# Kernel tuning notes

Hardware: AMD Instinct MI355X
Metric: run time of the kernel (lower is better)

## Reference

```python
import jax, jax.numpy as jnp
import numpy as np

B, N, E, D, F_IN, EDGE_DIM, VN = 128, 500, 1048576, 128, 5, 2, 10
NEG_FEAT = 0.01   # torch F.leaky_relu default
NEG_ATT = 0.2     # GAT attention slope


def _gat_layer(h_in, src, dst, edge_attr, W, b, a_src, a_dst, a_edge, We, n_nodes):
    # Edge-feature GAT conv: per-edge attention over (src, dst, edge) then
    # softmax-normalized scatter-aggregate onto destination nodes.
    h = h_in @ W                                  # [N, d]
    e = edge_attr @ We                            # [E, d] projected edge features
    logits = jax.nn.leaky_relu((h @ a_src)[src] + (h @ a_dst)[dst] + e @ a_edge,
                               negative_slope=NEG_ATT)    # [E]
    # segment softmax over incoming edges of each dst node
    m = jax.ops.segment_max(logits, dst, num_segments=n_nodes)
    ex = jnp.exp(logits - m[dst])
    denom = jax.ops.segment_sum(ex, dst, num_segments=n_nodes)
    alpha = ex / (denom[dst] + 1e-16)             # [E]
    msg = h[src] + e                              # [E, d]
    out = jax.ops.segment_sum(alpha[:, None] * msg, dst, num_segments=n_nodes)
    return out + b


def setup_inputs() -> dict:
    key = jax.random.key(0)
    ks = jax.random.split(key, 20)
    s = 0.05
    return {
        'x': jax.random.normal(ks[0], (B * N, F_IN), jnp.float32),
        'edge_index': jax.random.randint(ks[1], (2, E), 0, B * N, jnp.int64 if jax.config.jax_enable_x64 else jnp.int32).astype(jnp.int32),
        'edge_attr': jax.random.uniform(ks[2], (E, EDGE_DIM), jnp.float32),
        'curr_v_node_id': jax.random.randint(ks[3], (B,), 0, VN).astype(jnp.int32),
        'v_graph_embedding': jax.random.normal(ks[4], (B, D), jnp.float32),
        'v_node_dense_embeddings': jax.random.normal(ks[5], (B, VN, D), jnp.float32),
        'p_W': jax.random.normal(ks[6], (F_IN, D), jnp.float32) * s,
        'p_b': jnp.zeros((D,), jnp.float32),
        'Ws': jax.random.normal(ks[7], (4, D, D), jnp.float32) * s,
        'bs': jnp.zeros((4, D), jnp.float32),
        'a_srcs': jax.random.normal(ks[8], (4, D), jnp.float32) * s,
        'a_dsts': jax.random.normal(ks[9], (4, D), jnp.float32) * s,
        'a_edges': jax.random.normal(ks[10], (4, D), jnp.float32) * s,
        'Wes': jax.random.normal(ks[11], (4, EDGE_DIM, D), jnp.float32) * s,
        'W5': jax.random.normal(ks[12], (D, 1), jnp.float32) * s,
        'b5': jnp.zeros((1,), jnp.float32),
        'a_src5': jax.random.normal(ks[13], (1,), jnp.float32) * s,
        'a_dst5': jax.random.normal(ks[14], (1,), jnp.float32) * s,
        'a_edge5': jax.random.normal(ks[15], (1,), jnp.float32) * s,
        'We5': jax.random.normal(ks[16], (EDGE_DIM, 1), jnp.float32) * s,
    }


def reference(x, edge_index, edge_attr, curr_v_node_id, v_graph_embedding,
              v_node_dense_embeddings, p_W, p_b, Ws, bs, a_srcs, a_dsts,
              a_edges, Wes, W5, b5, a_src5, a_dst5, a_edge5, We5):
    n_nodes = x.shape[0]
    src, dst = edge_index[0], edge_index[1]
    # gather current v-node embedding: [B, D]
    curr_emb = v_node_dense_embeddings[jnp.arange(B), curr_v_node_id]
    # linear + leaky_relu then broadcast-add of graph/node context
    h = jax.nn.leaky_relu(x @ p_W + p_b, negative_slope=NEG_FEAT)  # [B*N, D]
    h = h.reshape(B, N, D) + v_graph_embedding[:, None, :] + curr_emb[:, None, :]
    h = h.reshape(B * N, D)
    # 4 hidden edge-feature GAT layers (128 -> 128) with leaky_relu
    for l in range(4):
        h = _gat_layer(h, src, dst, edge_attr, Ws[l], bs[l], a_srcs[l],
                       a_dsts[l], a_edges[l], Wes[l], n_nodes)
        h = jax.nn.leaky_relu(h, negative_slope=NEG_FEAT)
    # output layer (128 -> 1), no activation
    h = _gat_layer(h, src, dst, edge_attr, W5, b5, a_src5, a_dst5, a_edge5,
                   We5, n_nodes)                    # [B*N, 1]
    return h.reshape(B, N)
```

## Files before the change

### kernel.cpp

```cpp
#include <hip/hip_runtime.h>
#include <hip/hip_bf16.h>

#define BB   128
#define NN   500
#define NV   64000
#define EE   1048576
#define DD   128
#define FIN  5
#define VNN  10
#define NBUK 250
#define BCAP 8192

typedef unsigned int   uint32;
typedef unsigned short u16b;
typedef __attribute__((ext_vector_type(8))) short short8;
typedef __attribute__((ext_vector_type(4))) float float4v;

#define P_ASRC  0
#define P_ADST  512
#define P_WE    1024
#define P_BIAS  2048
#define P_W5    2560
#define P_CVEC  2688
#define P_SC5   2700
#define P_TOT   2816

static __device__ __forceinline__ float bf2f(__hip_bfloat16 v) { return __bfloat162float(v); }
static __device__ __forceinline__ float lo2f(uint32 u) { return __uint_as_float(u << 16); }
static __device__ __forceinline__ float hi2f(uint32 u) { return __uint_as_float(u & 0xFFFF0000u); }
static __device__ __forceinline__ uint32 f2bf_bits(float f) {
    uint32 u = __float_as_uint(f);
    return (u + 0x7FFFu + ((u >> 16) & 1u)) >> 16;
}
static __device__ __forceinline__ uint32 pack2(float a, float b) {
    return (f2bf_bits(a) & 0xFFFFu) | (f2bf_bits(b) << 16);
}
static __device__ __forceinline__ float ldf(const void* p, int i, int flag) {
    return flag ? ((const float*)p)[i] : bf2f(((const __hip_bfloat16*)p)[i]);
}

__global__ void sniff_kernel(const unsigned short* __restrict__ p16, int* __restrict__ FLAG) {
    __shared__ int sHigh, sZero;
    if (threadIdx.x == 0) { sHigh = 0; sZero = 0; }
    __syncthreads();
    unsigned short v = p16[2 * threadIdx.x];
    if (v >= 0x8000u) atomicOr(&sHigh, 1);
    if (v == 0)       atomicAdd(&sZero, 1);
    __syncthreads();
    if (threadIdx.x == 0) FLAG[0] = (sHigh || sZero >= 128) ? 1 : 0;
}

__global__ void zero_out_kernel(void* __restrict__ out, const int* __restrict__ FLAG, float tag) {
    int i = blockIdx.x * blockDim.x + threadIdx.x;
    if (i >= NV) return;
    float v = (i == 0) ? tag : 0.f;
    if (FLAG[0]) ((float*)out)[i] = v;
    else         ((u16b*)out)[i] = (u16b)f2bf_bits(v);
}

__global__ void prep_kernel(const void* __restrict__ Wes, const void* __restrict__ aeg,
                            const void* __restrict__ We5, const void* __restrict__ ae5,
                            const void* __restrict__ asr, const void* __restrict__ ads,
                            const void* __restrict__ bs, const void* __restrict__ W5,
                            const void* __restrict__ b5, const void* __restrict__ as5,
                            const void* __restrict__ ad5, const int* __restrict__ FLAG,
                            float* __restrict__ PAR) {
    const int flag = FLAG[0];
    if (blockIdx.x == 0) {
        for (int i = threadIdx.x; i < 512; i += 256) PAR[P_ASRC + i] = ldf(asr, i, flag);
    } else if (blockIdx.x == 1) {
        for (int i = threadIdx.x; i < 512; i += 256) PAR[P_ADST + i] = ldf(ads, i, flag);
    } else if (blockIdx.x == 2) {
        for (int i = threadIdx.x; i < 1024; i += 256) PAR[P_WE + i] = ldf(Wes, i, flag);
    } else if (blockIdx.x == 3) {
        for (int i = threadIdx.x; i < 512; i += 256) PAR[P_BIAS + i] = ldf(bs, i, flag);
    } else if (blockIdx.x == 4) {
        int tid = threadIdx.x;
        if (tid < 128) {
            PAR[P_W5 + tid] = ldf(W5, tid, flag);
        } else if (tid < 136) {
            int l = (tid - 128) >> 1, r = (tid - 128) & 1;
            float s = 0.f;
            for (int ch = 0; ch < DD; ++ch)
                s += ldf(Wes, l * 256 + r * DD + ch, flag) * ldf(aeg, l * DD + ch, flag);
            PAR[P_CVEC + l * 2 + r] = s;
        } else if (tid == 136) {
            float ae = ldf(ae5, 0, flag);
            float w0 = ldf(We5, 0, flag), w1 = ldf(We5, 1, flag);
            PAR[P_CVEC + 8] = w0 * ae; PAR[P_CVEC + 9] = w1 * ae;
            PAR[P_CVEC + 10] = w0;     PAR[P_CVEC + 11] = w1;
            PAR[P_SC5 + 0] = ldf(b5, 0, flag);
            PAR[P_SC5 + 1] = ldf(as5, 0, flag);
            PAR[P_SC5 + 2] = ldf(ad5, 0, flag);
        }
    }
}

__global__ __launch_bounds__(256) void prepack_kernel(const void* __restrict__ Ws,
                                                      const int* __restrict__ FLAG,
                                                      u16b* __restrict__ WB) {
    const int flag = FLAG[0];
    int t = blockIdx.x * 256 + threadIdx.x;
    int lane = t & 63;
    int frag = t >> 6;
    int nchunk = frag & 7, kblk = (frag >> 3) & 3, l = frag >> 5;
    int n = nchunk * 16 + (lane & 15);
    int kbase = kblk * 32 + (lane >> 4) * 8;
#pragma unroll
    for (int j = 0; j < 8; ++j) {
        int idx = l * 16384 + (kbase + j) * 128 + n;
        u16b bits = flag ? (u16b)f2bf_bits(((const float*)Ws)[idx])
                         : ((const u16b*)Ws)[idx];
        WB[(size_t)t * 8 + j] = bits;
    }
}

__global__ __launch_bounds__(256) void proj_kernel(
        const void* __restrict__ x, const void* __restrict__ pW,
        const void* __restrict__ pb, const int* __restrict__ curr,
        const void* __restrict__ vge, const void* __restrict__ vnd,
        const int* __restrict__ FLAG, uint32* __restrict__ H) {
    const int flag = FLAG[0];
    const int n = blockIdx.x * 4 + (threadIdx.x >> 6);
    const int lane = threadIdx.x & 63;
    const int b = n / NN;
    int cv = curr[b]; if ((unsigned)cv >= VNN) cv = 0;
    float xv[FIN];
#pragma unroll
    for (int k = 0; k < FIN; ++k) xv[k] = ldf(x, n * FIN + k, flag);
    const int ch = lane * 2;
    float s0 = ldf(pb, ch, flag), s1 = ldf(pb, ch + 1, flag);
#pragma unroll
    for (int k = 0; k < FIN; ++k) {
        s0 = fmaf(xv[k], ldf(pW, k * DD + ch, flag), s0);
        s1 = fmaf(xv[k], ldf(pW, k * DD + ch + 1, flag), s1);
    }
    s0 = (s0 > 0.f) ? s0 : 0.01f * s0;
    s1 = (s1 > 0.f) ? s1 : 0.01f * s1;
    s0 += ldf(vge, b * DD + ch, flag) + ldf(vnd, (b * VNN + cv) * DD + ch, flag);
    s1 += ldf(vge, b * DD + ch + 1, flag) + ldf(vnd, (b * VNN + cv) * DD + ch + 1, flag);
    H[(size_t)n * 64 + lane] = pack2(s0, s1);
}

__global__ void init_kernel(int* __restrict__ gcur, int* __restrict__ counts) {
    int t = blockIdx.x * 256 + threadIdx.x;
    if (t < NBUK) gcur[t] = t * BCAP;
    if (t < 512) counts[NV + t] = 0;
}

__global__ __launch_bounds__(256) void bucketize_kernel(
        const int* __restrict__ src, const int* __restrict__ dst,
        const void* __restrict__ eaP, const int* __restrict__ FLAG,
        int* __restrict__ gcur, uint32* __restrict__ bukx, uint32* __restrict__ buky) {
    __shared__ int cnt[256];
    __shared__ int cur[256];
    const int flag = FLAG[0];
    const int t = threadIdx.x;
    const int e0 = blockIdx.x * 4096;
    cnt[t] = 0;
    __syncthreads();
    int d[16];
#pragma unroll
    for (int i = 0; i < 16; ++i) {
        d[i] = dst[e0 + i * 256 + t];
        if ((unsigned)d[i] >= NV) d[i] = -1;
        if (d[i] >= 0) atomicAdd(&cnt[d[i] >> 8], 1);
    }
    __syncthreads();
    if (t < NBUK) {
        int c = cnt[t];
        cur[t] = c ? atomicAdd(&gcur[t], c) : 0;
    }
    __syncthreads();
#pragma unroll
    for (int i = 0; i < 16; ++i) {
        if (d[i] < 0) continue;
        int e = e0 + i * 256 + t;
        int b = d[i] >> 8;
        int s = src[e];
        if ((unsigned)s >= NV) s = 0;
        uint32 eb;
        if (flag) { float2 v = ((const float2*)eaP)[e]; eb = pack2(v.x, v.y); }
        else      eb = ((const uint32*)eaP)[e];
        int p = atomicAdd(&cur[b], 1);
        if (p < (b + 1) * BCAP) {
            bukx[p] = (uint32)((s & 0xFFFF) | ((d[i] & 255) << 16));
            buky[p] = eb;
        }
    }
}

__global__ __launch_bounds__(256) void bcount_kernel(
        const uint32* __restrict__ bukx, const int* __restrict__ gcur,
        int* __restrict__ counts) {
    __shared__ int c[256];
    const int b = blockIdx.x, t = threadIdx.x;
    c[t] = 0;
    __syncthreads();
    const int base = b * BCAP;
    int cnt = gcur[b] - base;
    if (cnt > BCAP) cnt = BCAP;
    for (int i = t; i < cnt; i += 256)
        atomicAdd(&c[(bukx[base + i] >> 16) & 255], 1);
    __syncthreads();
    counts[b * 256 + t] = c[t];
}

__global__ __launch_bounds__(256) void scan1_kernel(const int* __restrict__ counts,
                                                    int* __restrict__ row_ptr,
                                                    int* __restrict__ partials) {
    __shared__ int sdata[256];
    int tid = threadIdx.x;
    int4 v = ((const int4*)counts)[blockIdx.x * 256 + tid];
    int sum = v.x + v.y + v.z + v.w;
    sdata[tid] = sum;
    __syncthreads();
    int acc = sum;
    for (int off = 1; off < 256; off <<= 1) {
        int t = (tid >= off) ? sdata[tid - off] : 0;
        __syncthreads();
        acc += t;
        sdata[tid] = acc;
        __syncthreads();
    }
    int excl = acc - sum;
    int base = blockIdx.x * 1024 + tid * 4;
    int run = excl;
    if (base + 0 <= NV) row_ptr[base + 0] = run; run += v.x;
    if (base + 1 <= NV) row_ptr[base + 1] = run; run += v.y;
    if (base + 2 <= NV) row_ptr[base + 2] = run; run += v.z;
    if (base + 3 <= NV) row_ptr[base + 3] = run;
    if (tid == 255) partials[blockIdx.x] = acc;
}

__global__ __launch_bounds__(64) void scan2_kernel(const int* __restrict__ partials,
                                                   int* __restrict__ boff, int nb) {
    int lane = threadIdx.x;
    int v = (lane < nb) ? partials[lane] : 0;
    int orig = v;
#pragma unroll
    for (int off = 1; off < 64; off <<= 1) {
        int t = __shfl_up(v, off, 64);
        if (lane >= off) v += t;
    }
    boff[lane] = v - orig;
}

__global__ __launch_bounds__(256) void scan3_kernel(int* __restrict__ row_ptr,
                                                    const int* __restrict__ boff) {
    int add = boff[blockIdx.x];
    int base = blockIdx.x * 1024 + threadIdx.x * 4;
#pragma unroll
    for (int j = 0; j < 4; ++j) {
        int i = base + j;
        if (i <= NV) row_ptr[i] += add;
    }
}

__global__ __launch_bounds__(256) void bscatter_kernel(
        const uint32* __restrict__ bukx, const uint32* __restrict__ buky,
        const int* __restrict__ gcur, const int* __restrict__ row_ptr,
        int* __restrict__ csr_src, uint32* __restrict__ csr_ea) {
    __shared__ int cur[256];
    const int b = blockIdx.x, t = threadIdx.x;
    cur[t] = row_ptr[b * 256 + t];
    __syncthreads();
    const int base = b * BCAP;
    int cnt = gcur[b] - base;
    if (cnt > BCAP) cnt = BCAP;
    for (int i = t; i < cnt; i += 256) {
        uint32 x = bukx[base + i];
        uint32 y = buky[base + i];
        int p = atomicAdd(&cur[(x >> 16) & 255], 1);
        csr_src[p] = (int)(x & 0xFFFFu);
        csr_ea[p] = y;
    }
}

__global__ __launch_bounds__(256) void gemm_kernel(
        const uint32* __restrict__ Hu, const u16b* __restrict__ WBl,
        const float* __restrict__ PARl, uint32* __restrict__ HWu,
        float* __restrict__ ssrc, float* __restrict__ sdst) {
    __shared__ float hs[64 * 129];
    __shared__ float pp[512];
    const int tid = threadIdx.x;
    const int lane = tid & 63;
    const int wave = tid >> 6;
    const int quad = lane >> 4;
    const int n0 = blockIdx.x * 64;
    const int m = n0 + wave * 16 + (lane & 15);

    const u16b* hrow = (const u16b*)Hu + (size_t)m * 128;
    short8 a0 = *(const short8*)(hrow + 0  + quad * 8);
    short8 a1 = *(const short8*)(hrow + 32 + quad * 8);
    short8 a2 = *(const short8*)(hrow + 64 + quad * 8);
    short8 a3 = *(const short8*)(hrow + 96 + quad * 8);

#pragma unroll
    for (int nt = 0; nt < 8; ++nt) {
        const u16b* bbase = WBl + ((size_t)nt * 512 + lane * 8);
        short8 b0 = *(const short8*)(bbase + 0 * 4096);
        short8 b1 = *(const short8*)(bbase + 1 * 4096);
        short8 b2 = *(const short8*)(bbase + 2 * 4096);
        short8 b3 = *(const short8*)(bbase + 3 * 4096);
        float4v acc = {0.f, 0.f, 0.f, 0.f};
        acc = __builtin_amdgcn_mfma_f32_16x16x32_bf16(a0, b0, acc, 0, 0, 0);
        acc = __builtin_amdgcn_mfma_f32_16x16x32_bf16(a1, b1, acc, 0, 0, 0);
        acc = __builtin_amdgcn_mfma_f32_16x16x32_bf16(a2, b2, acc, 0, 0, 0);
        acc = __builtin_amdgcn_mfma_f32_16x16x32_bf16(a3, b3, acc, 0, 0, 0);
#pragma unroll
        for (int r = 0; r < 4; ++r)
            hs[(wave * 16 + quad * 4 + r) * 129 + nt * 16 + (lane & 15)] = acc[r];
    }
    __syncthreads();

    {
        const int mn = tid & 63, cg = tid >> 6;
        const float* Asr = PARl + P_ASRC;
        const float* Ads = PARl + P_ADST;
        const float* row = hs + mn * 129 + cg * 32;
        float ps = 0.f, pd = 0.f;
#pragma unroll
        for (int j = 0; j < 32; ++j) {
            float v = row[j];
            ps = fmaf(v, Asr[cg * 32 + j], ps);
            pd = fmaf(v, Ads[cg * 32 + j], pd);
        }
        pp[tid] = ps; pp[256 + tid] = pd;
    }
    __syncthreads();
    if (tid < 64) {
        ssrc[n0 + tid] = pp[tid] + pp[64 + tid] + pp[128 + tid] + pp[192 + tid];
        sdst[n0 + tid] = pp[256 + tid] + pp[320 + tid] + pp[384 + tid] + pp[448 + tid];
    }

#pragma unroll
    for (int i = 0; i < 4; ++i) {
        int flat = i * 2048 + tid * 8;
        int n = flat >> 7, c = flat & 127;
        const float* p = hs + n * 129 + c;
        uint4 v;
        v.x = pack2(p[0], p[1]); v.y = pack2(p[2], p[3]);
        v.z = pack2(p[4], p[5]); v.w = pack2(p[6], p[7]);
        *(uint4*)(HWu + (size_t)(n0 + n) * 64 + c / 2) = v;
    }
}

__global__ __launch_bounds__(256) void agg_kernel(
        const uint32* __restrict__ HWu, const float* __restrict__ ssrc,
        const float* __restrict__ sdst, const int* __restrict__ csr_src,
        const uint32* __restrict__ csr_ea, const int* __restrict__ row_ptr,
        const float* __restrict__ PAR, int layer, uint32* __restrict__ HoutU,
        float* __restrict__ hw5out, int wantw5) {
    const int lane = threadIdx.x & 63;
    const int n = blockIdx.x * 4 + (threadIdx.x >> 6);
    const int begin = __builtin_amdgcn_readfirstlane(row_ptr[n]);
    const int deg   = __builtin_amdgcn_readfirstlane(row_ptr[n + 1]) - begin;
    const float c0 = PAR[P_CVEC + 2 * layer], c1 = PAR[P_CVEC + 2 * layer + 1];
    const float sd = sdst[n];

    int   sv = 0;
    uint32 eb = 0;
    float L = -3.4e38f;
    if (lane < deg) {
        sv = csr_src[begin + lane];
        eb = csr_ea[begin + lane];
        L = fmaf(hi2f(eb), c1, fmaf(lo2f(eb), c0, ssrc[sv] + sd));
        L = (L > 0.f) ? L : 0.2f * L;
    }
    float m = L;
    for (int j0 = 64; j0 < deg; j0 += 64) {
        int j = j0 + lane;
        if (j < deg) {
            int s2 = csr_src[begin + j];
            uint32 e2 = csr_ea[begin + j];
            float L2 = fmaf(hi2f(e2), c1, fmaf(lo2f(e2), c0, ssrc[s2] + sd));
            L2 = (L2 > 0.f) ? L2 : 0.2f * L2;
            m = fmaxf(m, L2);
        }
    }
#pragma unroll
    for (int o = 32; o; o >>= 1) m = fmaxf(m, __shfl_xor(m, o, 64));

    float ex = (lane < deg) ? __expf(L - m) : 0.f;
    float dsum = ex, sx = ex * lo2f(eb), sy = ex * hi2f(eb);
    for (int j0 = 64; j0 < deg; j0 += 64) {
        int j = j0 + lane;
        if (j < deg) {
            int s2 = csr_src[begin + j];
            uint32 e2 = csr_ea[begin + j];
            float L2 = fmaf(hi2f(e2), c1, fmaf(lo2f(e2), c0, ssrc[s2] + sd));
            L2 = (L2 > 0.f) ? L2 : 0.2f * L2;
            float x2 = __expf(L2 - m);
            dsum += x2; sx = fmaf(x2, lo2f(e2), sx); sy = fmaf(x2, hi2f(e2), sy);
        }
    }
#pragma unroll
    for (int o = 32; o; o >>= 1) {
        dsum += __shfl_xor(dsum, o, 64);
        sx   += __shfl_xor(sx, o, 64);
        sy   += __shfl_xor(sy, o, 64);
    }

    const int dmain = (deg < 64) ? deg : 64;
    const uint32 exu = __float_as_uint(ex);
    float acc0 = 0.f, acc1 = 0.f;
    int jj = 0;
    for (; jj + 8 <= dmain; jj += 8) {
        int s8[8]; float e8[8]; uint32 hv[8];
#pragma unroll
        for (int q = 0; q < 8; ++q) {
            s8[q] = __builtin_amdgcn_readlane(sv, jj + q);
            e8[q] = __uint_as_float(__builtin_amdgcn_readlane((int)exu, jj + q));
        }
#pragma unroll
        for (int q = 0; q < 8; ++q) hv[q] = HWu[(size_t)s8[q] * 64 + lane];
#pragma unroll
        for (int q = 0; q < 8; ++q) {
            acc0 = fmaf(e8[q], lo2f(hv[q]), acc0);
            acc1 = fmaf(e8[q], hi2f(hv[q]), acc1);
        }
    }
    for (; jj < dmain; ++jj) {
        int s = __builtin_amdgcn_readlane(sv, jj);
        float e1v = __uint_as_float(__builtin_amdgcn_readlane((int)exu, jj));
        uint32 hb = HWu[(size_t)s * 64 + lane];
        acc0 = fmaf(e1v, lo2f(hb), acc0);
        acc1 = fmaf(e1v, hi2f(hb), acc1);
    }
    for (jj = 64; jj < deg; ++jj) {
        int s = csr_src[begin + jj];
        uint32 e2 = csr_ea[begin + jj];
        float L2 = fmaf(hi2f(e2), c1, fmaf(lo2f(e2), c0, ssrc[s] + sd));
        L2 = (L2 > 0.f) ? L2 : 0.2f * L2;
        float x2 = __expf(L2 - m);
        uint32 hb = HWu[(size_t)s * 64 + lane];
        acc0 = fmaf(x2, lo2f(hb), acc0);
        acc1 = fmaf(x2, hi2f(hb), acc1);
    }

    const int ch = lane * 2;
    const float* WEl = PAR + P_WE + layer * 256;
    const float inv = 1.f / (dsum + 1e-16f);
    const float* Bl = PAR + P_BIAS + layer * DD;
    float t0 = fmaf(sy, WEl[DD + ch],     fmaf(sx, WEl[ch],     acc0));
    float t1 = fmaf(sy, WEl[DD + ch + 1], fmaf(sx, WEl[ch + 1], acc1));
    float o0 = fmaf(t0, inv, Bl[ch]);
    float o1 = fmaf(t1, inv, Bl[ch + 1]);
    o0 = (o0 > 0.f) ? o0 : 0.01f * o0;
    o1 = (o1 > 0.f) ? o1 : 0.01f * o1;
    HoutU[(size_t)n * 64 + lane] = pack2(o0, o1);

    if (wantw5) {
        float p = o0 * PAR[P_W5 + ch] + o1 * PAR[P_W5 + ch + 1];
#pragma unroll
        for (int o = 32; o; o >>= 1) p += __shfl_xor(p, o, 64);
        if (lane == 0) hw5out[n] = p;
    }
}

__global__ __launch_bounds__(256) void final_kernel(
        const float* __restrict__ hw5, const int* __restrict__ csr_src,
        const uint32* __restrict__ csr_ea, const int* __restrict__ row_ptr,
        const float* __restrict__ PAR, const int* __restrict__ FLAG,
        void* __restrict__ out) {
    const int flag = FLAG[0];
    int lane = threadIdx.x & 63;
    int n = blockIdx.x * 4 + (threadIdx.x >> 6);
    int begin = __builtin_amdgcn_readfirstlane(row_ptr[n]);
    int deg   = __builtin_amdgcn_readfirstlane(row_ptr[n + 1]) - begin;
    float c50 = PAR[P_CVEC + 8], c51 = PAR[P_CVEC + 9];
    float ce0 = PAR[P_CVEC + 10], ce1 = PAR[P_CVEC + 11];
    float b5v = PAR[P_SC5], a5s = PAR[P_SC5 + 1];
    float hd = PAR[P_SC5 + 2] * hw5[n];

    float m = -3.4e38f;
    for (int j0 = 0; j0 < deg; j0 += 64) {
        int j = j0 + lane;
        if (j < deg) {
            int s = csr_src[begin + j];
            uint32 eb = csr_ea[begin + j];
            float L = fmaf(hi2f(eb), c51, fmaf(lo2f(eb), c50, fmaf(a5s, hw5[s], hd)));
            L = (L > 0.f) ? L : 0.2f * L;
            m = fmaxf(m, L);
        }
    }
#pragma unroll
    for (int o = 32; o; o >>= 1) m = fmaxf(m, __shfl_xor(m, o, 64));

    float dsum = 0.f, msum = 0.f;
    for (int j0 = 0; j0 < deg; j0 += 64) {
        int j = j0 + lane;
        if (j < deg) {
            int s = csr_src[begin + j];
            uint32 eb = csr_ea[begin + j];
            float hs5 = hw5[s];
            float L = fmaf(hi2f(eb), c51, fmaf(lo2f(eb), c50, fmaf(a5s, hs5, hd)));
            L = (L > 0.f) ? L : 0.2f * L;
            float ex = __expf(L - m);
            dsum += ex;
            msum = fmaf(ex, hs5 + fmaf(hi2f(eb), ce1, lo2f(eb) * ce0), msum);
        }
    }
#pragma unroll
    for (int o = 32; o; o >>= 1) {
        dsum += __shfl_xor(dsum, o, 64);
        msum += __shfl_xor(msum, o, 64);
    }
    if (lane == 0) {
        float r = msum / (dsum + 1e-16f) + b5v;
        if (flag) ((float*)out)[n] = r;
        else      ((u16b*)out)[n] = (u16b)f2bf_bits(r);
    }
}

extern "C" void kernel_launch(void* const* d_in, const int* in_sizes, int n_in,
                              void* d_out, int out_size, void* d_ws, size_t ws_size,
                              hipStream_t stream) {
    const void* x   = d_in[0];
    const int*  ei  = (const int*)d_in[1];
    const void* ea  = d_in[2];
    const int*  cur = (const int*)d_in[3];
    const void* vge = d_in[4];
    const void* vnd = d_in[5];
    const void* pW  = d_in[6];
    const void* pb  = d_in[7];
    const void* Ws  = d_in[8];
    const void* bs  = d_in[9];
    const void* asr = d_in[10];
    const void* ads = d_in[11];
    const void* aeg = d_in[12];
    const void* Wes = d_in[13];
    const void* W5  = d_in[14];
    const void* b5  = d_in[15];
    const void* as5 = d_in[16];
    const void* ad5 = d_in[17];
    const void* ae5 = d_in[18];
    const void* We5 = d_in[19];
    (void)in_sizes; (void)n_in; (void)out_size;

    const int* e_src = ei;
    const int* e_dst = ei + EE;

    size_t off = 0;
    char* base = (char*)d_ws;
    auto carve = [&](size_t bytes) {
        void* p = base + off;
        off += (bytes + 255) & ~(size_t)255;
        return p;
    };
    int*    FLAG   = (int*)carve(256);
    float*  PAR    = (float*)carve((size_t)P_TOT * 4);
    u16b*   WB     = (u16b*)carve(4 * DD * DD * 2);
    uint32* H0     = (uint32*)carve((size_t)NV * DD * 2);
    uint32* H1     = (uint32*)carve((size_t)NV * DD * 2);
    float*  SS     = (float*)carve(NV * 4);
    float*  SD     = (float*)carve(NV * 4);
    float*  HW5v   = (float*)carve(NV * 4);
    int*    COUNTS = (int*)carve(65536 * 4);
    int*    ROWPTR = (int*)carve(65536 * 4);
    int*    GCUR   = (int*)carve(256 * 4);
    int*    PART   = (int*)carve(256 * 4);
    int*    BOFF   = (int*)carve(256 * 4);
    int*    CSRS   = (int*)carve((size_t)EE * 4);
    uint32* CSREA  = (uint32*)carve((size_t)EE * 4);
    size_t need = off;

    uint32* BUKX = H1;
    uint32* BUKY = H1 + (size_t)NBUK * BCAP;

    sniff_kernel<<<1, 256, 0, stream>>>((const unsigned short*)ea, FLAG);

    if (need > ws_size) {
        zero_out_kernel<<<(NV + 255) / 256, 256, 0, stream>>>(
            d_out, FLAG, (float)(ws_size >> 20));
        return;
    }

    prep_kernel<<<5, 256, 0, stream>>>(Wes, aeg, We5, ae5, asr, ads, bs,
                                       W5, b5, as5, ad5, FLAG, PAR);
    prepack_kernel<<<32, 256, 0, stream>>>(Ws, FLAG, WB);
    proj_kernel<<<NV / 4, 256, 0, stream>>>(x, pW, pb, cur, vge, vnd, FLAG, H0);

    init_kernel<<<2, 256, 0, stream>>>(GCUR, COUNTS);
    bucketize_kernel<<<EE / 4096, 256, 0, stream>>>(e_src, e_dst, ea, FLAG,
                                                    GCUR, BUKX, BUKY);
    bcount_kernel<<<NBUK, 256, 0, stream>>>(BUKX, GCUR, COUNTS);
    scan1_kernel<<<63, 256, 0, stream>>>(COUNTS, ROWPTR, PART);
    scan2_kernel<<<1, 64, 0, stream>>>(PART, BOFF, 63);
    scan3_kernel<<<63, 256, 0, stream>>>(ROWPTR, BOFF);
    bscatter_kernel<<<NBUK, 256, 0, stream>>>(BUKX, BUKY, GCUR, ROWPTR,
                                              CSRS, CSREA);

    for (int l = 0; l < 4; ++l) {
        gemm_kernel<<<NV / 64, 256, 0, stream>>>(
            H0, WB + (size_t)l * 16384, PAR + l * DD, H1, SS, SD);
        agg_kernel<<<NV / 4, 256, 0, stream>>>(
            H1, SS, SD, CSRS, CSREA, ROWPTR, PAR, l, H0, HW5v, (l == 3) ? 1 : 0);
    }

    final_kernel<<<NV / 4, 256, 0, stream>>>(HW5v, CSRS, CSREA, ROWPTR, PAR,
                                             FLAG, d_out);
}
```

Before: 464.6 us.

## Split GAT aggregation into attention and channel-sliced gather with sliced H layout

Hidden features are stored as 8 channel slices of 16 channels each, so every node row within a slice is 32 bytes. The fused aggregation kernel is split in two. An attention kernel computes the normalized alpha per edge, stores it as fp16 packed beside the source index, and writes the edge-attribute sums per node. A gather kernel launched per slice then reads 8 edges at a time with 8 lanes per edge. The intent is a smaller working set per slice for better cache hit rates on the random source gathers. In exchange it adds a kernel launch per layer, extra edge-array traffic, fp16 alpha precision loss, and atomics for hw5.

```diff
diff --git a/kernel.cpp b/kernel.cpp
--- a/kernel.cpp
+++ b/kernel.cpp
@@ -1,5 +1,6 @@
 #include <hip/hip_runtime.h>
 #include <hip/hip_bf16.h>
+#include <hip/hip_fp16.h>
 
 #define BB   128
 #define NN   500
@@ -25,6 +26,8 @@
 #define P_SC5   2700
 #define P_TOT   2816
 
+#define HIDXU(s, n, u) (((size_t)(s) * NV + (n)) * 8 + (u))
+
 static __device__ __forceinline__ float bf2f(__hip_bfloat16 v) { return __bfloat162float(v); }
 static __device__ __forceinline__ float lo2f(uint32 u) { return __uint_as_float(u << 16); }
 static __device__ __forceinline__ float hi2f(uint32 u) { return __uint_as_float(u & 0xFFFF0000u); }
@@ -37,6 +40,9 @@
 }
 static __device__ __forceinline__ float ldf(const void* p, int i, int flag) {
     return flag ? ((const float*)p)[i] : bf2f(((const __hip_bfloat16*)p)[i]);
+}
+static __device__ __forceinline__ float a2f(uint32 al) {
+    return __half2float(__ushort_as_half((unsigned short)(al >> 16)));
 }
 
 __global__ void sniff_kernel(const unsigned short* __restrict__ p16, int* __restrict__ FLAG) {
@@ -139,7 +145,7 @@
     s1 = (s1 > 0.f) ? s1 : 0.01f * s1;
     s0 += ldf(vge, b * DD + ch, flag) + ldf(vnd, (b * VNN + cv) * DD + ch, flag);
     s1 += ldf(vge, b * DD + ch + 1, flag) + ldf(vnd, (b * VNN + cv) * DD + ch + 1, flag);
-    H[(size_t)n * 64 + lane] = pack2(s0, s1);
+    H[HIDXU(lane >> 3, n, lane & 7)] = pack2(s0, s1);
 }
 
 __global__ void init_kernel(int* __restrict__ gcur, int* __restrict__ counts) {
@@ -260,7 +266,7 @@
 __global__ __launch_bounds__(256) void bscatter_kernel(
         const uint32* __restrict__ bukx, const uint32* __restrict__ buky,
         const int* __restrict__ gcur, const int* __restrict__ row_ptr,
-        int* __restrict__ csr_src, uint32* __restrict__ csr_ea) {
+        uint32* __restrict__ e1, uint32* __restrict__ csr_ea) {
     __shared__ int cur[256];
     const int b = blockIdx.x, t = threadIdx.x;
     cur[t] = row_ptr[b * 256 + t];
@@ -272,7 +278,7 @@
         uint32 x = bukx[base + i];
         uint32 y = buky[base + i];
         int p = atomicAdd(&cur[(x >> 16) & 255], 1);
-        csr_src[p] = (int)(x & 0xFFFFu);
+        e1[p] = x & 0xFFFFu;
         csr_ea[p] = y;
     }
 }
@@ -290,11 +296,11 @@
     const int n0 = blockIdx.x * 64;
     const int m = n0 + wave * 16 + (lane & 15);
 
-    const u16b* hrow = (const u16b*)Hu + (size_t)m * 128;
-    short8 a0 = *(const short8*)(hrow + 0  + quad * 8);
-    short8 a1 = *(const short8*)(hrow + 32 + quad * 8);
-    short8 a2 = *(const short8*)(hrow + 64 + quad * 8);
-    short8 a3 = *(const short8*)(hrow + 96 + quad * 8);
+    const int sA = quad >> 1, uA = (quad & 1) * 4;
+    short8 a0 = *(const short8*)(Hu + HIDXU(0 + sA, m, uA));
+    short8 a1 = *(const short8*)(Hu + HIDXU(2 + sA, m, uA));
+    short8 a2 = *(const short8*)(Hu + HIDXU(4 + sA, m, uA));
+    short8 a3 = *(const short8*)(Hu + HIDXU(6 + sA, m, uA));
 
 #pragma unroll
     for (int nt = 0; nt < 8; ++nt) {
@@ -335,23 +341,19 @@
     }
 
 #pragma unroll
-    for (int i = 0; i < 4; ++i) {
-        int flat = i * 2048 + tid * 8;
-        int n = flat >> 7, c = flat & 127;
-        const float* p = hs + n * 129 + c;
-        uint4 v;
-        v.x = pack2(p[0], p[1]); v.y = pack2(p[2], p[3]);
-        v.z = pack2(p[4], p[5]); v.w = pack2(p[6], p[7]);
-        *(uint4*)(HWu + (size_t)(n0 + n) * 64 + c / 2) = v;
-    }
-}
-
-__global__ __launch_bounds__(256) void agg_kernel(
-        const uint32* __restrict__ HWu, const float* __restrict__ ssrc,
-        const float* __restrict__ sdst, const int* __restrict__ csr_src,
-        const uint32* __restrict__ csr_ea, const int* __restrict__ row_ptr,
-        const float* __restrict__ PAR, int layer, uint32* __restrict__ HoutU,
-        float* __restrict__ hw5out, int wantw5) {
+    for (int it = 0; it < 16; ++it) {
+        int f = it * 256 + tid;
+        int u = f & 7, n = (f >> 3) & 63, s = f >> 9;
+        const float* p = hs + n * 129 + s * 16 + u * 2;
+        HWu[HIDXU(s, n0 + n, u)] = pack2(p[0], p[1]);
+    }
+}
+
+__global__ __launch_bounds__(256) void attn_kernel(
+        const float* __restrict__ ssrc, const float* __restrict__ sdst,
+        uint32* __restrict__ e1, const uint32* __restrict__ csr_ea,
+        const int* __restrict__ row_ptr, const float* __restrict__ PAR,
+        int layer, float2* __restrict__ SXY) {
     const int lane = threadIdx.x & 63;
     const int n = blockIdx.x * 4 + (threadIdx.x >> 6);
     const int begin = __builtin_amdgcn_readfirstlane(row_ptr[n]);
@@ -359,22 +361,20 @@
     const float c0 = PAR[P_CVEC + 2 * layer], c1 = PAR[P_CVEC + 2 * layer + 1];
     const float sd = sdst[n];
 
-    int   sv = 0;
-    uint32 eb = 0;
+    uint32 ev = 0, eb = 0;
     float L = -3.4e38f;
     if (lane < deg) {
-        sv = csr_src[begin + lane];
+        ev = e1[begin + lane];
         eb = csr_ea[begin + lane];
-        L = fmaf(hi2f(eb), c1, fmaf(lo2f(eb), c0, ssrc[sv] + sd));
+        L = fmaf(hi2f(eb), c1, fmaf(lo2f(eb), c0, ssrc[ev & 0xFFFFu] + sd));
         L = (L > 0.f) ? L : 0.2f * L;
     }
     float m = L;
     for (int j0 = 64; j0 < deg; j0 += 64) {
         int j = j0 + lane;
         if (j < deg) {
-            int s2 = csr_src[begin + j];
-            uint32 e2 = csr_ea[begin + j];
-            float L2 = fmaf(hi2f(e2), c1, fmaf(lo2f(e2), c0, ssrc[s2] + sd));
+            uint32 e2 = e1[begin + j], b2 = csr_ea[begin + j];
+            float L2 = fmaf(hi2f(b2), c1, fmaf(lo2f(b2), c0, ssrc[e2 & 0xFFFFu] + sd));
             L2 = (L2 > 0.f) ? L2 : 0.2f * L2;
             m = fmaxf(m, L2);
         }
@@ -387,12 +387,11 @@
     for (int j0 = 64; j0 < deg; j0 += 64) {
         int j = j0 + lane;
         if (j < deg) {
-            int s2 = csr_src[begin + j];
-            uint32 e2 = csr_ea[begin + j];
-            float L2 = fmaf(hi2f(e2), c1, fmaf(lo2f(e2), c0, ssrc[s2] + sd));
+            uint32 e2 = e1[begin + j], b2 = csr_ea[begin + j];
+            float L2 = fmaf(hi2f(b2), c1, fmaf(lo2f(b2), c0, ssrc[e2 & 0xFFFFu] + sd));
             L2 = (L2 > 0.f) ? L2 : 0.2f * L2;
             float x2 = __expf(L2 - m);
-            dsum += x2; sx = fmaf(x2, lo2f(e2), sx); sy = fmaf(x2, hi2f(e2), sy);
+            dsum += x2; sx = fmaf(x2, lo2f(b2), sx); sy = fmaf(x2, hi2f(b2), sy);
         }
     }
 #pragma unroll
@@ -401,66 +400,74 @@
         sx   += __shfl_xor(sx, o, 64);
         sy   += __shfl_xor(sy, o, 64);
     }
-
-    const int dmain = (deg < 64) ? deg : 64;
-    const uint32 exu = __float_as_uint(ex);
+    const float inv = 1.f / (dsum + 1e-16f);
+    if (lane < deg) {
+        uint32 ah = (uint32)__half_as_ushort(__float2half(ex * inv));
+        e1[begin + lane] = (ev & 0xFFFFu) | (ah << 16);
+    }
+    for (int j0 = 64; j0 < deg; j0 += 64) {
+        int j = j0 + lane;
+        if (j < deg) {
+            uint32 e2 = e1[begin + j], b2 = csr_ea[begin + j];
+            float L2 = fmaf(hi2f(b2), c1, fmaf(lo2f(b2), c0, ssrc[e2 & 0xFFFFu] + sd));
+            L2 = (L2 > 0.f) ? L2 : 0.2f * L2;
+            uint32 ah = (uint32)__half_as_ushort(__float2half(__expf(L2 - m) * inv));
+            e1[begin + j] = (e2 & 0xFFFFu) | (ah << 16);
+        }
+    }
+    if (lane == 0) SXY[n] = make_float2(sx * inv, sy * inv);
+}
+
+__global__ __launch_bounds__(256) void gather_kernel(
+        const uint32* __restrict__ HWs, const uint32* __restrict__ e1,
+        const float2* __restrict__ SXY, const int* __restrict__ row_ptr,
+        const float* __restrict__ PAR, int layer, uint32* __restrict__ Hout,
+        float* __restrict__ hw5, int wantw5) {
+    const int s = blockIdx.x & 7;
+    const int n = (blockIdx.x >> 3) * 4 + (threadIdx.x >> 6);
+    const int lane = threadIdx.x & 63;
+    const int g = lane >> 3, u = lane & 7;
+    const int begin = __builtin_amdgcn_readfirstlane(row_ptr[n]);
+    const int deg   = __builtin_amdgcn_readfirstlane(row_ptr[n + 1]) - begin;
+
+    const uint32* rowb = HWs + (size_t)s * NV * 8;
     float acc0 = 0.f, acc1 = 0.f;
-    int jj = 0;
-    for (; jj + 8 <= dmain; jj += 8) {
-        int s8[8]; float e8[8]; uint32 hv[8];
-#pragma unroll
-        for (int q = 0; q < 8; ++q) {
-            s8[q] = __builtin_amdgcn_readlane(sv, jj + q);
-            e8[q] = __uint_as_float(__builtin_amdgcn_readlane((int)exu, jj + q));
-        }
-#pragma unroll
-        for (int q = 0; q < 8; ++q) hv[q] = HWu[(size_t)s8[q] * 64 + lane];
-#pragma unroll
-        for (int q = 0; q < 8; ++q) {
-            acc0 = fmaf(e8[q], lo2f(hv[q]), acc0);
-            acc1 = fmaf(e8[q], hi2f(hv[q]), acc1);
-        }
-    }
-    for (; jj < dmain; ++jj) {
-        int s = __builtin_amdgcn_readlane(sv, jj);
-        float e1v = __uint_as_float(__builtin_amdgcn_readlane((int)exu, jj));
-        uint32 hb = HWu[(size_t)s * 64 + lane];
-        acc0 = fmaf(e1v, lo2f(hb), acc0);
-        acc1 = fmaf(e1v, hi2f(hb), acc1);
-    }
-    for (jj = 64; jj < deg; ++jj) {
-        int s = csr_src[begin + jj];
-        uint32 e2 = csr_ea[begin + jj];
-        float L2 = fmaf(hi2f(e2), c1, fmaf(lo2f(e2), c0, ssrc[s] + sd));
-        L2 = (L2 > 0.f) ? L2 : 0.2f * L2;
-        float x2 = __expf(L2 - m);
-        uint32 hb = HWu[(size_t)s * 64 + lane];
-        acc0 = fmaf(x2, lo2f(hb), acc0);
-        acc1 = fmaf(x2, hi2f(hb), acc1);
-    }
-
-    const int ch = lane * 2;
+    for (int j0 = 0; j0 < deg; j0 += 8) {
+        int e = j0 + g;
+        int ec = (e < deg) ? e : (deg - 1);
+        uint32 al = __builtin_nontemporal_load(&e1[begin + ec]);
+        float a = (e < deg) ? a2f(al) : 0.f;
+        uint32 hv = rowb[(size_t)(al & 0xFFFFu) * 8 + u];
+        acc0 = fmaf(a, lo2f(hv), acc0);
+        acc1 = fmaf(a, hi2f(hv), acc1);
+    }
+#pragma unroll
+    for (int o = 8; o < 64; o <<= 1) {
+        acc0 += __shfl_xor(acc0, o, 64);
+        acc1 += __shfl_xor(acc1, o, 64);
+    }
+
+    const float2 sxy = SXY[n];
+    const int ch = s * 16 + u * 2;
     const float* WEl = PAR + P_WE + layer * 256;
-    const float inv = 1.f / (dsum + 1e-16f);
-    const float* Bl = PAR + P_BIAS + layer * DD;
-    float t0 = fmaf(sy, WEl[DD + ch],     fmaf(sx, WEl[ch],     acc0));
-    float t1 = fmaf(sy, WEl[DD + ch + 1], fmaf(sx, WEl[ch + 1], acc1));
-    float o0 = fmaf(t0, inv, Bl[ch]);
-    float o1 = fmaf(t1, inv, Bl[ch + 1]);
+    const float* Bl  = PAR + P_BIAS + layer * DD;
+    float o0 = acc0 + sxy.x * WEl[ch]     + sxy.y * WEl[DD + ch]     + Bl[ch];
+    float o1 = acc1 + sxy.x * WEl[ch + 1] + sxy.y * WEl[DD + ch + 1] + Bl[ch + 1];
     o0 = (o0 > 0.f) ? o0 : 0.01f * o0;
     o1 = (o1 > 0.f) ? o1 : 0.01f * o1;
-    HoutU[(size_t)n * 64 + lane] = pack2(o0, o1);
+    if (g == 0)
+        __builtin_nontemporal_store(pack2(o0, o1), &Hout[HIDXU(s, n, u)]);
 
     if (wantw5) {
-        float p = o0 * PAR[P_W5 + ch] + o1 * PAR[P_W5 + ch + 1];
+        float p = (g == 0) ? (o0 * PAR[P_W5 + ch] + o1 * PAR[P_W5 + ch + 1]) : 0.f;
 #pragma unroll
         for (int o = 32; o; o >>= 1) p += __shfl_xor(p, o, 64);
-        if (lane == 0) hw5out[n] = p;
+        if (lane == 0) atomicAdd(&hw5[n], p);
     }
 }
 
 __global__ __launch_bounds__(256) void final_kernel(
-        const float* __restrict__ hw5, const int* __restrict__ csr_src,
+        const float* __restrict__ hw5, const uint32* __restrict__ e1,
         const uint32* __restrict__ csr_ea, const int* __restrict__ row_ptr,
         const float* __restrict__ PAR, const int* __restrict__ FLAG,
         void* __restrict__ out) {
@@ -478,7 +485,7 @@
     for (int j0 = 0; j0 < deg; j0 += 64) {
         int j = j0 + lane;
         if (j < deg) {
-            int s = csr_src[begin + j];
+            int s = (int)(e1[begin + j] & 0xFFFFu);
             uint32 eb = csr_ea[begin + j];
             float L = fmaf(hi2f(eb), c51, fmaf(lo2f(eb), c50, fmaf(a5s, hw5[s], hd)));
             L = (L > 0.f) ? L : 0.2f * L;
@@ -492,7 +499,7 @@
     for (int j0 = 0; j0 < deg; j0 += 64) {
         int j = j0 + lane;
         if (j < deg) {
-            int s = csr_src[begin + j];
+            int s = (int)(e1[begin + j] & 0xFFFFu);
             uint32 eb = csr_ea[begin + j];
             float hs5 = hw5[s];
             float L = fmaf(hi2f(eb), c51, fmaf(lo2f(eb), c50, fmaf(a5s, hs5, hd)));
@@ -557,12 +564,13 @@
     float*  SS     = (float*)carve(NV * 4);
     float*  SD     = (float*)carve(NV * 4);
     float*  HW5v   = (float*)carve(NV * 4);
+    float2* SXY    = (float2*)carve((size_t)NV * 8);
     int*    COUNTS = (int*)carve(65536 * 4);
     int*    ROWPTR = (int*)carve(65536 * 4);
     int*    GCUR   = (int*)carve(256 * 4);
     int*    PART   = (int*)carve(256 * 4);
     int*    BOFF   = (int*)carve(256 * 4);
-    int*    CSRS   = (int*)carve((size_t)EE * 4);
+    uint32* E1     = (uint32*)carve((size_t)EE * 4);
     uint32* CSREA  = (uint32*)carve((size_t)EE * 4);
     size_t need = off;
 
@@ -590,15 +598,18 @@
     scan2_kernel<<<1, 64, 0, stream>>>(PART, BOFF, 63);
     scan3_kernel<<<63, 256, 0, stream>>>(ROWPTR, BOFF);
     bscatter_kernel<<<NBUK, 256, 0, stream>>>(BUKX, BUKY, GCUR, ROWPTR,
-                                              CSRS, CSREA);
+                                              E1, CSREA);
+    hipMemsetAsync(HW5v, 0, (size_t)NV * 4, stream);
 
     for (int l = 0; l < 4; ++l) {
         gemm_kernel<<<NV / 64, 256, 0, stream>>>(
             H0, WB + (size_t)l * 16384, PAR + l * DD, H1, SS, SD);
-        agg_kernel<<<NV / 4, 256, 0, stream>>>(
-            H1, SS, SD, CSRS, CSREA, ROWPTR, PAR, l, H0, HW5v, (l == 3) ? 1 : 0);
-    }
-
-    final_kernel<<<NV / 4, 256, 0, stream>>>(HW5v, CSRS, CSREA, ROWPTR, PAR,
+        attn_kernel<<<NV / 4, 256, 0, stream>>>(
+            SS, SD, E1, CSREA, ROWPTR, PAR, l, SXY);
+        gather_kernel<<<(NV / 4) * 8, 256, 0, stream>>>(
+            H1, E1, SXY, ROWPTR, PAR, l, H0, HW5v, (l == 3) ? 1 : 0);
+    }
+
+    final_kernel<<<NV / 4, 256, 0, stream>>>(HW5v, E1, CSREA, ROWPTR, PAR,
                                              FLAG, d_out);
 }
```

Measured after the change: 1.213 ms. +161.2%, slower.
